# Kernel optimization log

Hardware: AMD Instinct MI355X
Metric: run time of the kernel (lower is better)

## Reference

```python
import jax, jax.numpy as jnp
import numpy as np

K = 7        # kernel_size
G = 16       # groups
P = K // 2   # padding
EPS = 1e-5   # BatchNorm eps


def setup_inputs() -> dict:
    key = jax.random.key(0)
    ks = jax.random.split(key, 4)
    B, C, H, W = 8, 256, 64, 64
    CR = C // 4              # channels_reduced (reduction_ratio=4)
    KKG = K * K * G          # span output channels
    return {
        "x": jax.random.normal(ks[0], (B, C, H, W), jnp.float32),
        "v_reduce": jax.random.normal(ks[1], (CR, C), jnp.float32) * 0.05,
        "g_reduce": jnp.ones((CR,), jnp.float32),
        "b_reduce": jnp.zeros((CR,), jnp.float32),
        "bn_gamma": jnp.ones((CR,), jnp.float32),
        "bn_beta": jnp.zeros((CR,), jnp.float32),
        "bn_mean": jnp.zeros((CR,), jnp.float32),
        "bn_var": jnp.ones((CR,), jnp.float32),
        "v_span": jax.random.normal(ks[2], (KKG, CR), jnp.float32) * 0.05,
        "g_span": jnp.ones((KKG,), jnp.float32),
        "b_span": jnp.zeros((KKG,), jnp.float32),
    }


def _weight_norm(v, g):
    # weight_norm on a 1x1 conv: w_o = g_o * v_o / ||v_o||  (norm over in-channel dim)
    return v * (g / jnp.linalg.norm(v, axis=1))[:, None]


def reference(x, v_reduce, g_reduce, b_reduce, bn_gamma, bn_beta, bn_mean, bn_var,
              v_span, g_span, b_span):
    B, C, H, W = x.shape
    D = C // G  # group channel width

    # reduce: 1x1 conv (weight-normed) + BatchNorm (eval, running stats) + ReLU
    w_r = _weight_norm(v_reduce, g_reduce)
    r = jnp.einsum('oc,bchw->bohw', w_r, x) + b_reduce[:, None, None]
    scale = (bn_gamma / jnp.sqrt(bn_var + EPS))[:, None, None]
    r = jax.nn.relu((r - bn_mean[:, None, None]) * scale + bn_beta[:, None, None])

    # span: 1x1 conv -> per-pixel kernels, channel layout is (k j g)
    w_s = _weight_norm(v_span, g_span)
    ker = jnp.einsum('oc,bchw->bohw', w_s, r) + b_span[:, None, None]
    ker = ker.reshape(B, K, K, G, H, W).transpose(0, 3, 1, 2, 4, 5)
    ker = ker.reshape(B, G, K * K, H, W)  # (b, g, kk, h, w)

    # fused involution: avoid materializing the [B,G,D,K*K,H,W] unfold tensor.
    xp = jnp.pad(x, ((0, 0), (0, 0), (P, P), (P, P)))
    xp = xp.reshape(B, G, D, H + 2 * P, W + 2 * P)
    out = jnp.zeros((B, G, D, H, W), x.dtype)
    for ki in range(K):
        for kj in range(K):
            out = out + xp[:, :, :, ki:ki + H, kj:kj + W] * ker[:, :, ki * K + kj][:, :, None]
    return out.reshape(B, C, H, W)
```

## Files before the change

kernel.cpp:

```cpp
#include <hip/hip_runtime.h>

#define KS 7
#define NG 16
#define PAD 3
#define EPS 1e-5f
#define NB 8
#define NC 256
#define CR 64
#define NH 64
#define NW 64
#define HW 4096
#define HPAD 70
#define KK 49
#define ND 16

#define XT_G   ((size_t)HPAD * HPAD * ND)
#define XT_B   ((size_t)NG * XT_G)

__global__ __launch_bounds__(256) void k_pad_t(const float* __restrict__ x,
                                               float* __restrict__ xt) {
    int idx = blockIdx.x * 256 + threadIdx.x;
    int dq = idx & 3;
    int t = idx >> 2;
    int wp = t % HPAD;
    int t2 = t / HPAD;
    int hp = t2 % HPAD;
    int t3 = t2 / HPAD;
    int g = t3 % NG;
    int b = t3 / NG;

    float4 v = make_float4(0.f, 0.f, 0.f, 0.f);
    int h = hp - PAD, w = wp - PAD;
    if (h >= 0 && h < NH && w >= 0 && w < NW) {
        const float* src = x + ((size_t)(b * NC + g * ND + dq * 4) * HW) + h * NW + w;
        v.x = src[0 * HW];
        v.y = src[1 * HW];
        v.z = src[2 * HW];
        v.w = src[3 * HW];
    }
    float4* dst = (float4*)(xt + (size_t)b * XT_B + (size_t)g * XT_G
                            + ((size_t)hp * HPAD + wp) * ND);
    dst[dq] = v;
}

__global__ __launch_bounds__(64) void k_prep(
    const float* __restrict__ v_reduce, const float* __restrict__ g_reduce,
    const float* __restrict__ b_reduce, const float* __restrict__ bn_gamma,
    const float* __restrict__ bn_beta, const float* __restrict__ bn_mean,
    const float* __restrict__ bn_var, const float* __restrict__ v_span,
    const float* __restrict__ g_span, const float* __restrict__ b_span,
    float* __restrict__ wrT, float* __restrict__ br,
    float* __restrict__ wsT, float* __restrict__ bs) {
    int row = blockIdx.x;
    int t = threadIdx.x;
    if (row < CR) {
        int o = row;
        float s = 0.f;
        #pragma unroll
        for (int i = 0; i < 4; i++) {
            float v = v_reduce[o * NC + t + 64 * i];
            s += v * v;
        }
        #pragma unroll
        for (int m = 32; m >= 1; m >>= 1) s += __shfl_xor(s, m);
        float norm = sqrtf(s);
        float bnscale = bn_gamma[o] * rsqrtf(bn_var[o] + EPS);
        float wscale = g_reduce[o] / norm * bnscale;
        #pragma unroll
        for (int i = 0; i < 4; i++) {
            int c = t + 64 * i;
            wrT[c * CR + o] = v_reduce[o * NC + c] * wscale;
        }
        if (t == 0) br[o] = (b_reduce[o] - bn_mean[o]) * bnscale + bn_beta[o];
    } else {
        int o = row - CR;
        float v = v_span[o * CR + t];
        float s = v * v;
        #pragma unroll
        for (int m = 32; m >= 1; m >>= 1) s += __shfl_xor(s, m);
        float norm = sqrtf(s);
        float wscale = g_span[o] / norm;
        int kk = o / NG, g = o % NG;
        wsT[(g * CR + t) * KK + kk] = v * wscale;
        if (t == 0) bs[g * KK + kk] = b_span[o];
    }
}

__global__ __launch_bounds__(256) void k_reduce(const float* __restrict__ x,
                                                const float* __restrict__ wrT,
                                                const float* __restrict__ br,
                                                float* __restrict__ r) {
    int oc = blockIdx.y;
    int b = blockIdx.z;
    int p = blockIdx.x * 256 + threadIdx.x;
    const float* xb = x + (size_t)b * NC * HW + p;
    float acc[16];
    #pragma unroll
    for (int o = 0; o < 16; o++) acc[o] = 0.f;
    const float* w0 = wrT + oc * 16;
    #pragma unroll 4
    for (int c = 0; c < NC; c++) {
        float xv = xb[(size_t)c * HW];
        const float* wc = w0 + c * CR;
        #pragma unroll
        for (int o = 0; o < 16; o++) acc[o] += wc[o] * xv;
    }
    float* rb = r + (size_t)b * CR * HW + (size_t)oc * 16 * HW + p;
    const float* brp = br + oc * 16;
    #pragma unroll
    for (int o = 0; o < 16; o++) {
        float v = acc[o] + brp[o];
        rb[(size_t)o * HW] = fmaxf(v, 0.f);
    }
}

__global__ __launch_bounds__(256) void k_span_inv(const float* __restrict__ r,
                                                  const float* __restrict__ wsT,
                                                  const float* __restrict__ bs,
                                                  const float* __restrict__ xt,
                                                  float* __restrict__ out) {
    int chunk = blockIdx.x;
    int g = blockIdx.y;
    int b = blockIdx.z;
    int p = chunk * 256 + threadIdx.x;
    int h = p >> 6, w = p & 63;

    float kv[KK];
    const float* bsp = bs + g * KK;
    #pragma unroll
    for (int k = 0; k < KK; k++) kv[k] = bsp[k];
    const float* rb = r + (size_t)b * CR * HW + p;
    const float* wg = wsT + (size_t)g * CR * KK;
    #pragma unroll 2
    for (int c = 0; c < CR; c++) {
        float rv = rb[(size_t)c * HW];
        const float* wc = wg + c * KK;
        #pragma unroll
        for (int k = 0; k < KK; k++) kv[k] += wc[k] * rv;
    }

    const float* xg = xt + (size_t)b * XT_B + (size_t)g * XT_G;
    float* ob = out + (size_t)(b * NC + g * ND) * HW + p;
    #pragma unroll
    for (int half = 0; half < 2; half++) {
        int d0 = half * 8;
        float acc[8];
        #pragma unroll
        for (int j = 0; j < 8; j++) acc[j] = 0.f;
        #pragma unroll
        for (int ki = 0; ki < KS; ki++) {
            const float* xrow = xg + ((size_t)(h + ki) * HPAD + w) * ND + d0;
            #pragma unroll
            for (int kj = 0; kj < KS; kj++) {
                const float4* q = (const float4*)(xrow + kj * ND);
                float4 a = q[0];
                float4 c4 = q[1];
                float kvv = kv[ki * KS + kj];
                acc[0] += a.x * kvv;
                acc[1] += a.y * kvv;
                acc[2] += a.z * kvv;
                acc[3] += a.w * kvv;
                acc[4] += c4.x * kvv;
                acc[5] += c4.y * kvv;
                acc[6] += c4.z * kvv;
                acc[7] += c4.w * kvv;
            }
        }
        #pragma unroll
        for (int j = 0; j < 8; j++)
            ob[(size_t)(d0 + j) * HW] = acc[j];
    }
}

extern "C" void kernel_launch(void* const* d_in, const int* in_sizes, int n_in,
                              void* d_out, int out_size, void* d_ws, size_t ws_size,
                              hipStream_t stream) {
    const float* x        = (const float*)d_in[0];
    const float* v_reduce = (const float*)d_in[1];
    const float* g_reduce = (const float*)d_in[2];
    const float* b_reduce = (const float*)d_in[3];
    const float* bn_gamma = (const float*)d_in[4];
    const float* bn_beta  = (const float*)d_in[5];
    const float* bn_mean  = (const float*)d_in[6];
    const float* bn_var   = (const float*)d_in[7];
    const float* v_span   = (const float*)d_in[8];
    const float* g_span   = (const float*)d_in[9];
    const float* b_span   = (const float*)d_in[10];
    float* out = (float*)d_out;

    float* ws = (float*)d_ws;
    size_t off = 0;
    float* xt   = ws + off; off += (size_t)NB * XT_B;
    float* r    = ws + off; off += (size_t)NB * CR * HW;
    float* wrT  = ws + off; off += (size_t)NC * CR;
    float* br   = ws + off; off += CR;
    float* wsT  = ws + off; off += (size_t)NG * CR * KK;
    float* bs   = ws + off; off += (size_t)NG * KK;

    int padt_threads = NB * NG * HPAD * HPAD * 4;
    k_pad_t<<<padt_threads / 256, 256, 0, stream>>>(x, xt);
    k_prep<<<CR + KK * NG, 64, 0, stream>>>(v_reduce, g_reduce, b_reduce,
                                            bn_gamma, bn_beta, bn_mean, bn_var,
                                            v_span, g_span, b_span,
                                            wrT, br, wsT, bs);
    dim3 gr(HW / 256, 4, NB);
    k_reduce<<<gr, 256, 0, stream>>>(x, wrT, br, r);
    dim3 gs(HW / 256, NG, NB);
    k_span_inv<<<gs, 256, 0, stream>>>(r, wsT, bs, xt, out);
}
```

Measured before the change: 264.5 us.

## Compute span kernels with bf16 MFMA and stage them through LDS

The per-pixel span 1x1 conv in k_span_inv now runs as a bf16 MFMA (16x16x32) GEMM. The intermediate r is stored pixel-major as bf16, and the span weights are padded to 64 and converted to bf16. Kernel weights go through shared memory so that each thread computes 4 output channels for one pixel, instead of every thread redoing the 64x49 FMA loop in scalar fp32. This cuts the redundant scalar work and halves r traffic, at the cost of bf16 rounding in both r and the span weights.

```diff
diff --git a/kernel.cpp b/kernel.cpp
--- a/kernel.cpp
+++ b/kernel.cpp
@@ -1,4 +1,5 @@
 #include <hip/hip_runtime.h>
+#include <hip/hip_bf16.h>
 
 #define KS 7
 #define NG 16
@@ -17,6 +18,14 @@
 #define XT_G   ((size_t)HPAD * HPAD * ND)
 #define XT_B   ((size_t)NG * XT_G)
 
+typedef short bf16x8 __attribute__((ext_vector_type(8)));
+typedef float f32x4 __attribute__((ext_vector_type(4)));
+
+static __device__ __forceinline__ ushort f2bf(float v) {
+    __hip_bfloat16 hb = __float2bfloat16(v);
+    return *reinterpret_cast<ushort*>(&hb);
+}
+
 __global__ __launch_bounds__(256) void k_pad_t(const float* __restrict__ x,
                                                float* __restrict__ xt) {
     int idx = blockIdx.x * 256 + threadIdx.x;
@@ -50,7 +59,7 @@
     const float* __restrict__ bn_var, const float* __restrict__ v_span,
     const float* __restrict__ g_span, const float* __restrict__ b_span,
     float* __restrict__ wrT, float* __restrict__ br,
-    float* __restrict__ wsT, float* __restrict__ bs) {
+    ushort* __restrict__ ws2, float* __restrict__ bs) {
     int row = blockIdx.x;
     int t = threadIdx.x;
     if (row < CR) {
@@ -73,23 +82,29 @@
         }
         if (t == 0) br[o] = (b_reduce[o] - bn_mean[o]) * bnscale + bn_beta[o];
     } else {
-        int o = row - CR;
-        float v = v_span[o * CR + t];
-        float s = v * v;
-        #pragma unroll
-        for (int m = 32; m >= 1; m >>= 1) s += __shfl_xor(s, m);
-        float norm = sqrtf(s);
-        float wscale = g_span[o] / norm;
-        int kk = o / NG, g = o % NG;
-        wsT[(g * CR + t) * KK + kk] = v * wscale;
-        if (t == 0) bs[g * KK + kk] = b_span[o];
+        int o2 = row - CR;
+        int g = o2 >> 6, kk = o2 & 63;
+        ushort wv = 0;
+        float bval = 0.f;
+        if (kk < KK) {
+            int o = kk * NG + g;
+            float v = v_span[o * CR + t];
+            float s = v * v;
+            #pragma unroll
+            for (int m = 32; m >= 1; m >>= 1) s += __shfl_xor(s, m);
+            float w = v * (g_span[o] / sqrtf(s));
+            wv = f2bf(w);
+            bval = b_span[o];
+        }
+        ws2[(((size_t)g << 6) + kk) * 64 + t] = wv;
+        if (t == 0) bs[(g << 6) + kk] = bval;
     }
 }
 
 __global__ __launch_bounds__(256) void k_reduce(const float* __restrict__ x,
                                                 const float* __restrict__ wrT,
                                                 const float* __restrict__ br,
-                                                float* __restrict__ r) {
+                                                ushort* __restrict__ rt) {
     int oc = blockIdx.y;
     int b = blockIdx.z;
     int p = blockIdx.x * 256 + threadIdx.x;
@@ -105,71 +120,79 @@
         #pragma unroll
         for (int o = 0; o < 16; o++) acc[o] += wc[o] * xv;
     }
-    float* rb = r + (size_t)b * CR * HW + (size_t)oc * 16 * HW + p;
     const float* brp = br + oc * 16;
-    #pragma unroll
-    for (int o = 0; o < 16; o++) {
-        float v = acc[o] + brp[o];
-        rb[(size_t)o * HW] = fmaxf(v, 0.f);
-    }
-}
-
-__global__ __launch_bounds__(256) void k_span_inv(const float* __restrict__ r,
-                                                  const float* __restrict__ wsT,
+    uint pk[8];
+    #pragma unroll
+    for (int j = 0; j < 8; j++) {
+        float v0 = fmaxf(acc[2 * j] + brp[2 * j], 0.f);
+        float v1 = fmaxf(acc[2 * j + 1] + brp[2 * j + 1], 0.f);
+        pk[j] = (uint)f2bf(v0) | ((uint)f2bf(v1) << 16);
+    }
+    uint4* dst = (uint4*)(rt + (((size_t)b * HW + p) << 6) + (oc << 4));
+    dst[0] = make_uint4(pk[0], pk[1], pk[2], pk[3]);
+    dst[1] = make_uint4(pk[4], pk[5], pk[6], pk[7]);
+}
+
+__global__ __launch_bounds__(256) void k_span_inv(const ushort* __restrict__ rt,
+                                                  const ushort* __restrict__ ws2,
                                                   const float* __restrict__ bs,
                                                   const float* __restrict__ xt,
                                                   float* __restrict__ out) {
-    int chunk = blockIdx.x;
-    int g = blockIdx.y;
-    int b = blockIdx.z;
-    int p = chunk * 256 + threadIdx.x;
-    int h = p >> 6, w = p & 63;
-
-    float kv[KK];
-    const float* bsp = bs + g * KK;
-    #pragma unroll
-    for (int k = 0; k < KK; k++) kv[k] = bsp[k];
-    const float* rb = r + (size_t)b * CR * HW + p;
-    const float* wg = wsT + (size_t)g * CR * KK;
-    #pragma unroll 2
-    for (int c = 0; c < CR; c++) {
-        float rv = rb[(size_t)c * HW];
-        const float* wc = wg + c * KK;
-        #pragma unroll
-        for (int k = 0; k < KK; k++) kv[k] += wc[k] * rv;
-    }
-
-    const float* xg = xt + (size_t)b * XT_B + (size_t)g * XT_G;
-    float* ob = out + (size_t)(b * NC + g * ND) * HW + p;
-    #pragma unroll
-    for (int half = 0; half < 2; half++) {
-        int d0 = half * 8;
-        float acc[8];
-        #pragma unroll
-        for (int j = 0; j < 8; j++) acc[j] = 0.f;
-        #pragma unroll
-        for (int ki = 0; ki < KS; ki++) {
-            const float* xrow = xg + ((size_t)(h + ki) * HPAD + w) * ND + d0;
-            #pragma unroll
-            for (int kj = 0; kj < KS; kj++) {
-                const float4* q = (const float4*)(xrow + kj * ND);
-                float4 a = q[0];
-                float4 c4 = q[1];
-                float kvv = kv[ki * KS + kj];
-                acc[0] += a.x * kvv;
-                acc[1] += a.y * kvv;
-                acc[2] += a.z * kvv;
-                acc[3] += a.w * kvv;
-                acc[4] += c4.x * kvv;
-                acc[5] += c4.y * kvv;
-                acc[6] += c4.z * kvv;
-                acc[7] += c4.w * kvv;
-            }
-        }
-        #pragma unroll
-        for (int j = 0; j < 8; j++)
-            ob[(size_t)(d0 + j) * HW] = acc[j];
-    }
+    __shared__ float kv_lds[64][65];
+    int h = blockIdx.x, g = blockIdx.y, b = blockIdx.z;
+    int tid = threadIdx.x;
+    int lane = tid & 63, wv = tid >> 6;
+
+    int m = lane & 15, kb = lane >> 4;
+    const ushort* wg = ws2 + ((size_t)g << 12);
+    bf16x8 bfrag[4][2];
+    #pragma unroll
+    for (int n = 0; n < 4; n++)
+        #pragma unroll
+        for (int ks = 0; ks < 2; ks++)
+            bfrag[n][ks] = *(const bf16x8*)(wg + (((n * 16 + m) << 6) + ks * 32 + kb * 8));
+    f32x4 acc[4];
+    #pragma unroll
+    for (int n = 0; n < 4; n++) {
+        float bv = bs[(g << 6) + n * 16 + m];
+        acc[n] = (f32x4){bv, bv, bv, bv};
+    }
+    const ushort* ra = rt + ((((size_t)b << 12) + (h << 6) + (wv << 4) + m) << 6);
+    #pragma unroll
+    for (int ks = 0; ks < 2; ks++) {
+        bf16x8 afrag = *(const bf16x8*)(ra + ks * 32 + kb * 8);
+        #pragma unroll
+        for (int n = 0; n < 4; n++)
+            acc[n] = __builtin_amdgcn_mfma_f32_16x16x32_bf16(afrag, bfrag[n][ks], acc[n], 0, 0, 0);
+    }
+    #pragma unroll
+    for (int n = 0; n < 4; n++)
+        #pragma unroll
+        for (int ri = 0; ri < 4; ri++)
+            kv_lds[(wv << 4) + (kb << 2) + ri][n * 16 + m] = acc[n][ri];
+    __syncthreads();
+
+    int q = tid & 3, pl = tid >> 2;
+    const float* xg = xt + (size_t)b * XT_B + (size_t)g * XT_G + (q << 2);
+    float a0 = 0.f, a1 = 0.f, a2 = 0.f, a3 = 0.f;
+    #pragma unroll
+    for (int ki = 0; ki < KS; ki++) {
+        const float* xrow = xg + ((size_t)(h + ki) * HPAD + pl) * ND;
+        #pragma unroll
+        for (int kj = 0; kj < KS; kj++) {
+            float kvv = kv_lds[pl][ki * KS + kj];
+            float4 xv = *(const float4*)(xrow + kj * ND);
+            a0 += xv.x * kvv;
+            a1 += xv.y * kvv;
+            a2 += xv.z * kvv;
+            a3 += xv.w * kvv;
+        }
+    }
+    float* ob = out + (((size_t)(b * NC + (g << 4) + (q << 2))) << 12) + (h << 6) + pl;
+    ob[0] = a0;
+    ob[HW] = a1;
+    ob[2 * HW] = a2;
+    ob[3 * HW] = a3;
 }
 
 extern "C" void kernel_launch(void* const* d_in, const int* in_sizes, int n_in,
@@ -190,21 +213,21 @@
 
     float* ws = (float*)d_ws;
     size_t off = 0;
-    float* xt   = ws + off; off += (size_t)NB * XT_B;
-    float* r    = ws + off; off += (size_t)NB * CR * HW;
-    float* wrT  = ws + off; off += (size_t)NC * CR;
-    float* br   = ws + off; off += CR;
-    float* wsT  = ws + off; off += (size_t)NG * CR * KK;
-    float* bs   = ws + off; off += (size_t)NG * KK;
+    float* xt    = ws + off; off += (size_t)NB * XT_B;
+    ushort* rt   = (ushort*)(ws + off); off += (size_t)NB * HW * CR / 2;
+    float* wrT   = ws + off; off += (size_t)NC * CR;
+    float* br    = ws + off; off += CR;
+    ushort* ws2  = (ushort*)(ws + off); off += (size_t)NG * 64 * 64 / 2;
+    float* bs    = ws + off; off += (size_t)NG * 64;
 
     int padt_threads = NB * NG * HPAD * HPAD * 4;
     k_pad_t<<<padt_threads / 256, 256, 0, stream>>>(x, xt);
-    k_prep<<<CR + KK * NG, 64, 0, stream>>>(v_reduce, g_reduce, b_reduce,
+    k_prep<<<CR + NG * 64, 64, 0, stream>>>(v_reduce, g_reduce, b_reduce,
                                             bn_gamma, bn_beta, bn_mean, bn_var,
                                             v_span, g_span, b_span,
-                                            wrT, br, wsT, bs);
+                                            wrT, br, ws2, bs);
     dim3 gr(HW / 256, 4, NB);
-    k_reduce<<<gr, 256, 0, stream>>>(x, wrT, br, r);
-    dim3 gs(HW / 256, NG, NB);
-    k_span_inv<<<gs, 256, 0, stream>>>(r, wsT, bs, xt, out);
-}
+    k_reduce<<<gr, 256, 0, stream>>>(x, wrT, br, rt);
+    dim3 gs(NH, NG, NB);
+    k_span_inv<<<gs, 256, 0, stream>>>(rt, ws2, bs, xt, out);
+}
```

Measured after the change: 215.2 us. 18.6% less time.
